# Performance work log

Hardware: AMD Instinct MI355X
Metric: run time of the kernel (lower is better)

Reference implementation:

```python
import jax, jax.numpy as jnp
import numpy as np

B, N, K = 128, 512, 6      # graphs, nodes per graph, kNN neighbors
IN_FEAT, POS_DIM, H = 128, 3, 256
NB = B * N                  # total nodes
EPS_BN = 1e-5


def setup_inputs() -> dict:
    key = jax.random.key(0)
    ks = jax.random.split(key, 32)
    inp = {
        "x": jax.random.normal(ks[0], (NB, IN_FEAT), dtype=jnp.float32),
        "pos": jax.random.normal(ks[1], (NB, POS_DIM), dtype=jnp.float32) * 5.0,
    }
    d_in = IN_FEAT + POS_DIM
    def lin(k, fi, fo):
        s = 1.0 / np.sqrt(fi)
        return jax.random.uniform(k, (fi, fo), jnp.float32, -s, s)
    # GCN layers
    inp["W1"] = lin(ks[2], d_in, H); inp["b1"] = jnp.zeros((H,), jnp.float32)
    inp["W2"] = lin(ks[3], H, H);    inp["b2"] = jnp.zeros((H,), jnp.float32)
    inp["W3"] = lin(ks[4], H, H);    inp["b3"] = jnp.zeros((H,), jnp.float32)
    # BatchNorm (eval mode: running stats)
    for i, km, kv in [(1, ks[5], ks[6]), (2, ks[7], ks[8]), (3, ks[9], ks[10])]:
        inp[f"g{i}"]  = jnp.ones((H,), jnp.float32)
        inp[f"be{i}"] = jnp.zeros((H,), jnp.float32)
        inp[f"m{i}"]  = jax.random.normal(km, (H,), jnp.float32) * 0.1
        inp[f"v{i}"]  = jax.random.uniform(kv, (H,), jnp.float32, 0.5, 1.5)
    # attention gate, heads
    inp["gate_w"] = lin(ks[11], H, 1); inp["gate_b"] = jnp.zeros((1,), jnp.float32)
    inp["aff_w"]  = lin(ks[12], H, 1); inp["aff_b"]  = jnp.zeros((1,), jnp.float32)
    inp["rl_w1"]  = lin(ks[13], H, H); inp["rl_b1"]  = jnp.zeros((H,), jnp.float32)
    inp["rl_w2"]  = lin(ks[14], H, POS_DIM); inp["rl_b2"] = jnp.zeros((POS_DIM,), jnp.float32)
    return inp


def _knn_edges(pos):
    # torch_geometric knn_graph semantics: per-graph k nearest neighbors,
    # no self loops, edges (neighbor -> node).  batch = repeat(arange(B), N).
    p = pos.reshape(B, N, POS_DIM)
    sq = jnp.sum(p * p, axis=-1)                                  # [B,N]
    d2 = sq[:, :, None] + sq[:, None, :] - 2.0 * jnp.einsum("bnd,bmd->bnm", p, p)
    d2 = jnp.where(jnp.eye(N, dtype=bool)[None], jnp.inf, d2)     # exclude self
    _, idx = jax.lax.top_k(-d2, K)                                # [B,N,K] local nbr ids
    offs = (jnp.arange(B) * N)[:, None, None]
    src = (idx + offs).reshape(-1)                                # neighbor (source)
    dst = jnp.repeat(jnp.arange(NB), K)                           # target node
    return src, dst


def _gcn(h, W, b, src, dst):
    # GCNConv: add self loops, symmetric norm D^-1/2 (A+I) D^-1/2
    hw = h @ W                                                    # [NB,H]
    deg = jax.ops.segment_sum(jnp.ones_like(dst, jnp.float32), dst, num_segments=NB) + 1.0
    dis = jax.lax.rsqrt(deg)
    norm = dis[src] * dis[dst]                                    # [E]
    agg = jax.ops.segment_sum(hw[src] * norm[:, None], dst, num_segments=NB)
    agg = agg + hw * (1.0 / deg)[:, None]                          # self loop term
    return agg + b


def _bn(h, g, be, m, v):
    return (h - m) * (g * jax.lax.rsqrt(v + EPS_BN)) + be


def reference(x, pos, W1, b1, W2, b2, W3, b3,
              g1, be1, m1, v1, g2, be2, m2, v2, g3, be3, m3, v3,
              gate_w, gate_b, aff_w, aff_b, rl_w1, rl_b1, rl_w2, rl_b2):
    src, dst = _knn_edges(pos)
    h = jnp.concatenate([x, pos], axis=1)                          # [NB, in_feat+3]
    h = jax.nn.relu(_bn(_gcn(h, W1, b1, src, dst), g1, be1, m1, v1))
    h = jax.nn.relu(_bn(_gcn(h, W2, b2, src, dst), g2, be2, m2, v2))
    h = jax.nn.relu(_bn(_gcn(h, W3, b3, src, dst), g3, be3, m3, v3))
    # (dropout is identity in eval mode)
    gate = jax.nn.relu(h @ gate_w + gate_b)[:, 0]                  # [NB]
    attn = jax.nn.softmax(gate.reshape(B, N), axis=1)              # scatter_softmax over batch
    gemb = jnp.einsum("bn,bnh->bh", attn, h.reshape(B, N, H))      # scatter_add of weighted x
    affinity = gemb @ aff_w + aff_b                                # [B,1]
    pose = jax.nn.relu(gemb @ rl_w1 + rl_b1) @ rl_w2 + rl_b2        # [B,3]
    return affinity, pose
```

## Files before the change

### kernel.cpp

```cpp
#include <hip/hip_runtime.h>
#include <hip/hip_bf16.h>
#include <math.h>
#include <float.h>

#define NBG 128
#define NND 512
#define KNN 6
#define NB_TOT (NBG*NND)
#define HF 256
#define NSTEP1 5

typedef short bf16x8 __attribute__((ext_vector_type(8)));
typedef float f32x4 __attribute__((ext_vector_type(4)));

__device__ __forceinline__ int swzoff(int row, int kbyte) {
    return (row*64 + kbyte) ^ (((row>>1)&3)<<4);
}

__device__ __forceinline__ void split_store(const float* v, char* hi_p, char* lo_p) {
    bf16x8 hi, lo;
    #pragma unroll
    for (int j = 0; j < 8; ++j) {
        __hip_bfloat16 h = __float2bfloat16(v[j]);
        float hf = __bfloat162float(h);
        __hip_bfloat16 l = __float2bfloat16(v[j] - hf);
        hi[j] = *(short*)&h;
        lo[j] = *(short*)&l;
    }
    *(bf16x8*)hi_p = hi;
    *(bf16x8*)lo_p = lo;
}

__device__ __forceinline__ int xcd_swz(int bid, int grid) {
    return (bid & 7) * (grid >> 3) + (bid >> 3);
}

__global__ __launch_bounds__(256) void knn_kernel(const float* __restrict__ pos,
                                                  unsigned short* __restrict__ nbr)
{
    const int blk = blockIdx.x;
    const int g = blk >> 3;
    const int chunk = (blk & 7) * 64;
    const int tid = threadIdx.x;
    const int node = chunk + (tid >> 2);
    const int sub = tid & 3;

    __shared__ float4 p4[NND + (NND>>6)];
    const float* pg = pos + (size_t)g * NND * 3;
    for (int n = tid; n < NND; n += 256) {
        float x = pg[n*3+0], y = pg[n*3+1], z = pg[n*3+2];
        p4[n + (n>>6)] = make_float4(x, y, z, x*x + y*y + z*z);
    }
    __syncthreads();

    const float4 pi = p4[node + (node>>6)];
    const float m2x = -2.0f*pi.x, m2y = -2.0f*pi.y, m2z = -2.0f*pi.z;

    float bdA[KNN], bdB[KNN]; int biA[KNN], biB[KNN];
    #pragma unroll
    for (int q = 0; q < KNN; ++q) {
        bdA[q] = FLT_MAX; biA[q] = 0x7fffffff;
        bdB[q] = FLT_MAX; biB[q] = 0x7fffffff;
    }

    const int j0 = sub * 128;
    const float4* baseA = &p4[sub*130];
    const float4* baseB = &p4[sub*130 + 65];

    #pragma unroll 2
    for (int t = 0; t < 64; ++t) {
        int ja = j0 + t, jb = j0 + 64 + t;
        float4 pa = baseA[t];
        float4 pb = baseB[t];
        float da = fmaf(m2z, pa.z, fmaf(m2y, pa.y, fmaf(m2x, pa.x, pa.w)));
        float db = fmaf(m2z, pb.z, fmaf(m2y, pb.y, fmaf(m2x, pb.x, pb.w)));
        da = (ja == node) ? FLT_MAX : da;
        db = (jb == node) ? FLT_MAX : db;
        float ca = da; int ia = ja;
        float cb = db; int ib = jb;
        #pragma unroll
        for (int q = 0; q < KNN; ++q) {
            bool sa = ca < bdA[q];
            float t1 = sa ? ca : bdA[q]; float t2 = sa ? bdA[q] : ca;
            int   t3 = sa ? ia : biA[q]; int   t4 = sa ? biA[q] : ia;
            bdA[q] = t1; ca = t2; biA[q] = t3; ia = t4;
            bool sb = cb < bdB[q];
            float u1 = sb ? cb : bdB[q]; float u2 = sb ? bdB[q] : cb;
            int   u3 = sb ? ib : biB[q]; int   u4 = sb ? biB[q] : ib;
            bdB[q] = u1; cb = u2; biB[q] = u3; ib = u4;
        }
    }

    float ld[KNN]; int li[KNN];
    #pragma unroll
    for (int q = 0; q < KNN; ++q) {
        float ad = bdA[q], xd = bdB[KNN-1-q];
        int   ai = biA[q], xi = biB[KNN-1-q];
        bool t = (ad < xd) || (ad == xd && ai < xi);
        ld[q] = t ? ad : xd;
        li[q] = t ? ai : xi;
    }
    #pragma unroll
    for (int pass = 0; pass < KNN-1; ++pass)
        #pragma unroll
        for (int a = 0; a < KNN-1-pass; ++a) {
            int b = a+1;
            bool sw = (ld[b] < ld[a]) || (ld[b] == ld[a] && li[b] < li[a]);
            float td = sw ? ld[b] : ld[a]; float ud = sw ? ld[a] : ld[b];
            int   ti = sw ? li[b] : li[a]; int   ui = sw ? li[a] : li[b];
            ld[a] = td; li[a] = ti; ld[b] = ud; li[b] = ui;
        }

    #pragma unroll
    for (int mi = 0; mi < 2; ++mi) {
        const int mask = 1 << mi;
        float od[KNN]; int oi[KNN];
        #pragma unroll
        for (int q = 0; q < KNN; ++q) {
            od[q] = __shfl_xor(ld[q], mask);
            oi[q] = __shfl_xor(li[q], mask);
        }
        #pragma unroll
        for (int q = 0; q < KNN; ++q) {
            float ad = ld[q], xd = od[KNN-1-q];
            int   ai = li[q], xi = oi[KNN-1-q];
            bool t = (ad < xd) || (ad == xd && ai < xi);
            ld[q] = t ? ad : xd;
            li[q] = t ? ai : xi;
        }
        #pragma unroll
        for (int pass = 0; pass < KNN-1; ++pass)
            #pragma unroll
            for (int a = 0; a < KNN-1-pass; ++a) {
                int b = a+1;
                bool sw = (ld[b] < ld[a]) || (ld[b] == ld[a] && li[b] < li[a]);
                float td = sw ? ld[b] : ld[a]; float ud = sw ? ld[a] : ld[b];
                int   ti = sw ? li[b] : li[a]; int   ui = sw ? li[a] : li[b];
                ld[a] = td; li[a] = ti; ld[b] = ud; li[b] = ui;
            }
    }

    if (sub == 0) {
        int base = (g*NND + node)*KNN;
        #pragma unroll
        for (int q = 0; q < KNN; ++q) nbr[base+q] = (unsigned short)li[q];
    }
}

__global__ __launch_bounds__(256) void prew_kernel(const float* __restrict__ W,
                                                   int K, int nstep,
                                                   char* __restrict__ Wimg)
{
    int gid = blockIdx.x*256 + threadIdx.x;
    int per_nb = nstep*512;
    int nb = gid / per_nb;
    int r  = gid - nb*per_nb;
    int step = r >> 9;
    int r2 = r & 511;
    int cl = r2 >> 2;
    int kc = (r2 & 3) * 8;
    float v[8];
    #pragma unroll
    for (int j = 0; j < 8; ++j) {
        int gk = step*32 + kc + j;
        v[j] = (gk < K) ? W[(size_t)gk*256 + nb*128 + cl] : 0.f;
    }
    char* base = Wimg + (size_t)nb*nstep*16384 + (size_t)step*16384;
    int off = swzoff(cl, kc*2);
    split_store(v, base + off, base + 8192 + off);
}

__global__ __launch_bounds__(256) void agg_first(const float* __restrict__ x,
                                                 const float* __restrict__ pos,
                                                 const unsigned short* __restrict__ nbr,
                                                 char* __restrict__ Aimg)
{
    int gid = xcd_swz(blockIdx.x, gridDim.x)*256 + threadIdx.x;
    int i = gid / 20, ch = gid - i*20;
    const float rs = 1.0f/sqrtf(7.0f);
    const float c1 = rs*rs, c2 = 1.0f/7.0f;
    const int gbase = i & ~(NND-1);
    float v[8];
    if (ch < 16) {
        int jn[KNN];
        #pragma unroll
        for (int q = 0; q < KNN; ++q) jn[q] = gbase + nbr[i*KNN+q];
        const float4* x4 = (const float4*)x;
        int c4 = ch*2;
        float4 s0 = x4[(size_t)i*32 + c4], s1 = x4[(size_t)i*32 + c4 + 1];
        float a0=0,a1=0,a2=0,a3=0,b0=0,b1=0,b2=0,b3=0;
        #pragma unroll
        for (int q = 0; q < KNN; ++q) {
            float4 t0 = x4[(size_t)jn[q]*32 + c4];
            float4 t1 = x4[(size_t)jn[q]*32 + c4 + 1];
            a0+=t0.x; a1+=t0.y; a2+=t0.z; a3+=t0.w;
            b0+=t1.x; b1+=t1.y; b2+=t1.z; b3+=t1.w;
        }
        v[0]=a0*c1+s0.x*c2; v[1]=a1*c1+s0.y*c2; v[2]=a2*c1+s0.z*c2; v[3]=a3*c1+s0.w*c2;
        v[4]=b0*c1+s1.x*c2; v[5]=b1*c1+s1.y*c2; v[6]=b2*c1+s1.z*c2; v[7]=b3*c1+s1.w*c2;
    } else if (ch == 16) {
        int jn[KNN];
        #pragma unroll
        for (int q = 0; q < KNN; ++q) jn[q] = gbase + nbr[i*KNN+q];
        float ax=0, ay=0, az=0;
        #pragma unroll
        for (int q = 0; q < KNN; ++q) {
            ax += pos[(size_t)jn[q]*3+0];
            ay += pos[(size_t)jn[q]*3+1];
            az += pos[(size_t)jn[q]*3+2];
        }
        v[0] = ax*c1 + pos[(size_t)i*3+0]*c2;
        v[1] = ay*c1 + pos[(size_t)i*3+1]*c2;
        v[2] = az*c1 + pos[(size_t)i*3+2]*c2;
        v[3]=v[4]=v[5]=v[6]=v[7]=0.f;
    } else {
        #pragma unroll
        for (int j = 0; j < 8; ++j) v[j] = 0.f;
    }
    int mb = i >> 7, row = i & 127, step = ch >> 2, kbyte = (ch & 3)*16;
    char* base = Aimg + (size_t)mb*(NSTEP1*16384) + (size_t)step*16384;
    int off = swzoff(row, kbyte);
    split_store(v, base + off, base + 8192 + off);
}

__global__ __launch_bounds__(256) void agg_h(const float* __restrict__ h,
                                             const unsigned short* __restrict__ nbr,
                                             char* __restrict__ Aimg)
{
    int gid = xcd_swz(blockIdx.x, gridDim.x)*256 + threadIdx.x;
    int i = gid >> 5, ch = gid & 31;
    const float rs = 1.0f/sqrtf(7.0f);
    const float c1 = rs*rs, c2 = 1.0f/7.0f;
    const int gbase = i & ~(NND-1);
    int jn[KNN];
    #pragma unroll
    for (int q = 0; q < KNN; ++q) jn[q] = gbase + nbr[i*KNN+q];
    const float4* h4 = (const float4*)h;
    int c4 = ch*2;
    float4 s0 = h4[(size_t)i*64 + c4], s1 = h4[(size_t)i*64 + c4 + 1];
    float a0=0,a1=0,a2=0,a3=0,b0=0,b1=0,b2=0,b3=0;
    #pragma unroll
    for (int q = 0; q < KNN; ++q) {
        float4 t0 = h4[(size_t)jn[q]*64 + c4];
        float4 t1 = h4[(size_t)jn[q]*64 + c4 + 1];
        a0+=t0.x; a1+=t0.y; a2+=t0.z; a3+=t0.w;
        b0+=t1.x; b1+=t1.y; b2+=t1.z; b3+=t1.w;
    }
    float v[8];
    v[0]=a0*c1+s0.x*c2; v[1]=a1*c1+s0.y*c2; v[2]=a2*c1+s0.z*c2; v[3]=a3*c1+s0.w*c2;
    v[4]=b0*c1+s1.x*c2; v[5]=b1*c1+s1.y*c2; v[6]=b2*c1+s1.z*c2; v[7]=b3*c1+s1.w*c2;
    int mb = i >> 7, row = i & 127, step = ch >> 2, kbyte = (ch & 3)*16;
    char* base = Aimg + (size_t)mb*(8*16384) + (size_t)step*16384;
    int off = swzoff(row, kbyte);
    split_store(v, base + off, base + 8192 + off);
}

__global__ __launch_bounds__(256,4) void gemm_mfma(
    const char* __restrict__ Aimg, const char* __restrict__ Wimg, int nstep,
    const float* __restrict__ bias,
    const float* __restrict__ gam, const float* __restrict__ bet,
    const float* __restrict__ mu,  const float* __restrict__ var,
    float* __restrict__ out)
{
    __shared__ uint4 lds4[34816/16];
    char* lds  = (char*)lds4;
    char* Alds = lds;
    char* Wlds = lds + 16384;
    float* scs = (float*)(lds + 32768);
    float* shs = scs + 256;
    const int tid = threadIdx.x;
    const int lane = tid & 63, wave = tid >> 6;
    const int wm = wave >> 1, wn = wave & 1;
    const int mblk = blockIdx.x, nblk = blockIdx.y;

    if (tid < 256) {
        float s = gam[tid] / sqrtf(var[tid] + 1e-5f);
        scs[tid] = s;
        shs[tid] = bet[tid] + (bias[tid] - mu[tid]) * s;
    }

    const char* Ab = Aimg + (size_t)mblk * nstep * 16384;
    const char* Wb = Wimg + (size_t)nblk * nstep * 16384;

    const char* gbase; char* lbase;
    int soff;
    if (wave < 2) { gbase = Ab;  lbase = Alds; soff = wave*8192; }
    else          { gbase = Wb;  lbase = Wlds; soff = (wave-2)*8192; }

    f32x4 acc[4][4];
    #pragma unroll
    for (int m = 0; m < 4; ++m)
        #pragma unroll
        for (int n = 0; n < 4; ++n) acc[m][n] = (f32x4){0.f,0.f,0.f,0.f};

    for (int s = 0; s < nstep; ++s) {
        #pragma unroll
        for (int i = 0; i < 8; ++i) {
            int off = soff + i*1024;
            __builtin_amdgcn_global_load_lds(
                (const __attribute__((address_space(1))) void*)(gbase + (size_t)s*16384 + off + lane*16),
                (__attribute__((address_space(3))) void*)(lbase + off), 16, 0, 0);
        }
        __syncthreads();
        const int kb = (lane >> 4) * 16;
        bf16x8 ah[4], al[4];
        #pragma unroll
        for (int m = 0; m < 4; ++m) {
            int row = wm*64 + m*16 + (lane & 15);
            int off = swzoff(row, kb);
            ah[m] = *(const bf16x8*)(Alds + off);
            al[m] = *(const bf16x8*)(Alds + 8192 + off);
        }
        #pragma unroll
        for (int n = 0; n < 4; ++n) {
            int col = wn*64 + n*16 + (lane & 15);
            int off = swzoff(col, kb);
            bf16x8 bh = *(const bf16x8*)(Wlds + off);
            bf16x8 bl = *(const bf16x8*)(Wlds + 8192 + off);
            #pragma unroll
            for (int m = 0; m < 4; ++m) {
                acc[m][n] = __builtin_amdgcn_mfma_f32_16x16x32_bf16(ah[m], bh, acc[m][n], 0, 0, 0);
                acc[m][n] = __builtin_amdgcn_mfma_f32_16x16x32_bf16(al[m], bh, acc[m][n], 0, 0, 0);
                acc[m][n] = __builtin_amdgcn_mfma_f32_16x16x32_bf16(ah[m], bl, acc[m][n], 0, 0, 0);
            }
        }
        __syncthreads();
    }

    #pragma unroll
    for (int n = 0; n < 4; ++n) {
        int c = nblk*128 + wn*64 + n*16 + (lane & 15);
        float sc = scs[c], sh = shs[c];
        #pragma unroll
        for (int m = 0; m < 4; ++m) {
            int r0 = mblk*128 + wm*64 + m*16 + (lane >> 4)*4;
            #pragma unroll
            for (int q = 0; q < 4; ++q) {
                float v = acc[m][n][q]*sc + sh;
                out[(size_t)(r0+q)*256 + c] = fmaxf(v, 0.f);
            }
        }
    }
}

__global__ __launch_bounds__(256) void gate_kernel(const float* __restrict__ h3,
                                                   const float* __restrict__ gate_w,
                                                   const float* __restrict__ gate_b,
                                                   float* __restrict__ gate)
{
    const int lane = threadIdx.x & 63;
    const int gw = (blockIdx.x*256 + threadIdx.x) >> 6;
    float4 w4 = ((const float4*)gate_w)[lane];
    float gb = gate_b[0];
    #pragma unroll
    for (int it = 0; it < 4; ++it) {
        int r = gw + it*8192;
        float4 v = ((const float4*)(h3 + (size_t)r*HF))[lane];
        float s = v.x*w4.x + v.y*w4.y + v.z*w4.z + v.w*w4.w;
        #pragma unroll
        for (int o = 32; o > 0; o >>= 1) s += __shfl_xor(s, o, 64);
        if (lane == 0) gate[r] = fmaxf(s + gb, 0.f);
    }
}

__device__ __forceinline__ float blk_sum256(float v, volatile float* red)
{
    #pragma unroll
    for (int o = 32; o > 0; o >>= 1) v += __shfl_xor(v, o, 64);
    __syncthreads();
    if ((threadIdx.x & 63) == 0) red[threadIdx.x >> 6] = v;
    __syncthreads();
    return (red[0] + red[1]) + (red[2] + red[3]);
}

__global__ __launch_bounds__(256) void attn_kernel(const float* __restrict__ gate,
                                                   float* __restrict__ attn)
{
    int g = blockIdx.x, tid = threadIdx.x;
    __shared__ float red[4];
    float g0 = gate[g*NND + tid];
    float g1 = gate[g*NND + 256 + tid];
    float m = fmaxf(g0, g1);
    #pragma unroll
    for (int o = 32; o > 0; o >>= 1) m = fmaxf(m, __shfl_xor(m, o, 64));
    if ((tid & 63) == 0) red[tid >> 6] = m;
    __syncthreads();
    m = fmaxf(fmaxf(red[0], red[1]), fmaxf(red[2], red[3]));
    float e0 = expf(g0 - m), e1 = expf(g1 - m);
    float S = blk_sum256(e0 + e1, red);
    attn[g*NND + tid]       = e0 / S;
    attn[g*NND + 256 + tid] = e1 / S;
}

__global__ __launch_bounds__(256) void gemb_kernel(const float* __restrict__ h3,
                                                   const float* __restrict__ attn,
                                                   float* __restrict__ gembp)
{
    const int g = blockIdx.x, s = blockIdx.y;
    const int tid = threadIdx.x, lane = tid & 63, w = tid >> 6;
    __shared__ float at[128];
    __shared__ float red4[4][HF];
    if (tid < 128) at[tid] = attn[g*NND + s*128 + tid];
    __syncthreads();
    const float* hb = h3 + (size_t)(g*NND + s*128 + w*32) * HF;
    float4 acc = make_float4(0.f, 0.f, 0.f, 0.f);
    #pragma unroll 4
    for (int n = 0; n < 32; ++n) {
        float a = at[w*32 + n];
        float4 v = ((const float4*)(hb + (size_t)n*HF))[lane];
        acc.x = fmaf(a, v.x, acc.x); acc.y = fmaf(a, v.y, acc.y);
        acc.z = fmaf(a, v.z, acc.z); acc.w = fmaf(a, v.w, acc.w);
    }
    *(float4*)&red4[w][lane*4] = acc;
    __syncthreads();
    if (tid < HF) {
        float sum = (red4[0][tid] + red4[1][tid]) + (red4[2][tid] + red4[3][tid]);
        gembp[((size_t)s*NBG + g)*HF + tid] = sum;
    }
}

__global__ __launch_bounds__(256) void heads_kernel(
    const float* __restrict__ gembp,
    const float* __restrict__ aff_w,  const float* __restrict__ aff_b,
    const float* __restrict__ rl_w1,  const float* __restrict__ rl_b1,
    const float* __restrict__ rl_w2,  const float* __restrict__ rl_b2,
    float* __restrict__ out)
{
    int g = blockIdx.x, tid = threadIdx.x;
    __shared__ float gemb[HF];
    __shared__ float red[4];
    float acc = (gembp[((size_t)0*NBG + g)*HF + tid] + gembp[((size_t)1*NBG + g)*HF + tid])
              + (gembp[((size_t)2*NBG + g)*HF + tid] + gembp[((size_t)3*NBG + g)*HF + tid]);
    gemb[tid] = acc;
    __syncthreads();

    float sa = blk_sum256(acc * aff_w[tid], red);
    if (tid == 0) out[g] = sa + aff_b[0];

    float t = rl_b1[tid];
    #pragma unroll 4
    for (int k2 = 0; k2 < HF; ++k2)
        t = fmaf(gemb[k2], rl_w1[(size_t)k2*HF + tid], t);
    t = fmaxf(t, 0.f);
    float s0 = blk_sum256(t * rl_w2[(size_t)tid*3 + 0], red);
    if (tid == 0) out[128 + g*3 + 0] = s0 + rl_b2[0];
    float s1 = blk_sum256(t * rl_w2[(size_t)tid*3 + 1], red);
    if (tid == 0) out[128 + g*3 + 1] = s1 + rl_b2[1];
    float s2 = blk_sum256(t * rl_w2[(size_t)tid*3 + 2], red);
    if (tid == 0) out[128 + g*3 + 2] = s2 + rl_b2[2];
}

extern "C" void kernel_launch(void* const* d_in, const int* in_sizes, int n_in,
                              void* d_out, int out_size, void* d_ws, size_t ws_size,
                              hipStream_t stream)
{
    const float* x      = (const float*)d_in[0];
    const float* pos    = (const float*)d_in[1];
    const float* W1     = (const float*)d_in[2];
    const float* b1     = (const float*)d_in[3];
    const float* W2     = (const float*)d_in[4];
    const float* b2     = (const float*)d_in[5];
    const float* W3     = (const float*)d_in[6];
    const float* b3     = (const float*)d_in[7];
    const float* g1     = (const float*)d_in[8];
    const float* be1    = (const float*)d_in[9];
    const float* m1     = (const float*)d_in[10];
    const float* v1     = (const float*)d_in[11];
    const float* g2     = (const float*)d_in[12];
    const float* be2    = (const float*)d_in[13];
    const float* m2     = (const float*)d_in[14];
    const float* v2     = (const float*)d_in[15];
    const float* g3     = (const float*)d_in[16];
    const float* be3    = (const float*)d_in[17];
    const float* m3     = (const float*)d_in[18];
    const float* v3     = (const float*)d_in[19];
    const float* gate_w = (const float*)d_in[20];
    const float* gate_b = (const float*)d_in[21];
    const float* aff_w  = (const float*)d_in[22];
    const float* aff_b  = (const float*)d_in[23];
    const float* rl_w1  = (const float*)d_in[24];
    const float* rl_b1  = (const float*)d_in[25];
    const float* rl_w2  = (const float*)d_in[26];
    const float* rl_b2  = (const float*)d_in[27];
    float* out = (float*)d_out;

    char* wsb = (char*)d_ws;
    unsigned short* nbr = (unsigned short*)wsb;
    char* Wimg1 = wsb + 786432;
    char* Wimg2 = Wimg1 + (size_t)2*NSTEP1*16384;
    char* Wimg3 = Wimg2 + (size_t)2*8*16384;
    float* h    = (float*)(Wimg3 + (size_t)2*8*16384);
    char* Aimg  = (char*)(h + (size_t)NB_TOT*HF);
    float* gate  = (float*)Aimg;
    float* attn  = gate + NB_TOT;
    float* gembp = attn + NB_TOT;

    knn_kernel<<<NBG*8, 256, 0, stream>>>(pos, nbr);
    prew_kernel<<<(2*NSTEP1*512)/256, 256, 0, stream>>>(W1, 131, NSTEP1, Wimg1);
    prew_kernel<<<(2*8*512)/256, 256, 0, stream>>>(W2, 256, 8, Wimg2);
    prew_kernel<<<(2*8*512)/256, 256, 0, stream>>>(W3, 256, 8, Wimg3);

    agg_first<<<(NB_TOT*20)/256, 256, 0, stream>>>(x, pos, nbr, Aimg);
    gemm_mfma<<<dim3(NB_TOT/128, 2), 256, 0, stream>>>(Aimg, Wimg1, NSTEP1,
        b1, g1, be1, m1, v1, h);
    agg_h<<<(NB_TOT*32)/256, 256, 0, stream>>>(h, nbr, Aimg);
    gemm_mfma<<<dim3(NB_TOT/128, 2), 256, 0, stream>>>(Aimg, Wimg2, 8,
        b2, g2, be2, m2, v2, h);
    agg_h<<<(NB_TOT*32)/256, 256, 0, stream>>>(h, nbr, Aimg);
    gemm_mfma<<<dim3(NB_TOT/128, 2), 256, 0, stream>>>(Aimg, Wimg3, 8,
        b3, g3, be3, m3, v3, h);

    gate_kernel<<<2048, 256, 0, stream>>>(h, gate_w, gate_b, gate);
    attn_kernel<<<NBG, 256, 0, stream>>>(gate, attn);
    gemb_kernel<<<dim3(NBG, 4), 256, 0, stream>>>(h, attn, gembp);
    heads_kernel<<<NBG, 256, 0, stream>>>(gembp, aff_w, aff_b,
                                          rl_w1, rl_b1, rl_w2, rl_b2, out);
}
```

Baseline: 248.0 us.

## Split kNN search over more threads, merge weight-prep launches, fuse softmax into gemb

The kNN kernel now gives each node 8 threads scanning 64 candidates each instead of 4 threads scanning 128, with one extra shuffle-merge round, and launches twice as many blocks. The three weight-prep launches become a single kernel that picks its matrix from the block index. The attention softmax kernel is removed and each gemb block recomputes the per-graph softmax from the gate values before the weighted sum. This is meant to cut launch count and shorten the serial kNN loop, at the cost of repeating the softmax in four blocks per graph and an extra merge round.

```diff
diff --git a/kernel.cpp b/kernel.cpp
--- a/kernel.cpp
+++ b/kernel.cpp
@@ -39,11 +39,11 @@
                                                   unsigned short* __restrict__ nbr)
 {
     const int blk = blockIdx.x;
-    const int g = blk >> 3;
-    const int chunk = (blk & 7) * 64;
+    const int g = blk >> 4;
+    const int chunk = (blk & 15) * 32;
     const int tid = threadIdx.x;
-    const int node = chunk + (tid >> 2);
-    const int sub = tid & 3;
+    const int node = chunk + (tid >> 3);
+    const int sub = tid & 7;
 
     __shared__ float4 p4[NND + (NND>>6)];
     const float* pg = pos + (size_t)g * NND * 3;
@@ -63,15 +63,14 @@
         bdB[q] = FLT_MAX; biB[q] = 0x7fffffff;
     }
 
-    const int j0 = sub * 128;
-    const float4* baseA = &p4[sub*130];
-    const float4* baseB = &p4[sub*130 + 65];
+    const int j0 = sub * 64;
+    const float4* base = &p4[sub*65];
 
     #pragma unroll 2
-    for (int t = 0; t < 64; ++t) {
-        int ja = j0 + t, jb = j0 + 64 + t;
-        float4 pa = baseA[t];
-        float4 pb = baseB[t];
+    for (int t = 0; t < 32; ++t) {
+        int ja = j0 + t, jb = j0 + 32 + t;
+        float4 pa = base[t];
+        float4 pb = base[t + 32];
         float da = fmaf(m2z, pa.z, fmaf(m2y, pa.y, fmaf(m2x, pa.x, pa.w)));
         float db = fmaf(m2z, pb.z, fmaf(m2y, pb.y, fmaf(m2x, pb.x, pb.w)));
         da = (ja == node) ? FLT_MAX : da;
@@ -112,7 +111,7 @@
         }
 
     #pragma unroll
-    for (int mi = 0; mi < 2; ++mi) {
+    for (int mi = 0; mi < 3; ++mi) {
         const int mask = 1 << mi;
         float od[KNN]; int oi[KNN];
         #pragma unroll
@@ -141,17 +140,23 @@
     }
 
     if (sub == 0) {
-        int base = (g*NND + node)*KNN;
-        #pragma unroll
-        for (int q = 0; q < KNN; ++q) nbr[base+q] = (unsigned short)li[q];
-    }
-}
-
-__global__ __launch_bounds__(256) void prew_kernel(const float* __restrict__ W,
-                                                   int K, int nstep,
-                                                   char* __restrict__ Wimg)
-{
-    int gid = blockIdx.x*256 + threadIdx.x;
+        int base2 = (g*NND + node)*KNN;
+        #pragma unroll
+        for (int q = 0; q < KNN; ++q) nbr[base2+q] = (unsigned short)li[q];
+    }
+}
+
+__global__ __launch_bounds__(256) void prew_all(
+    const float* __restrict__ W1, const float* __restrict__ W2,
+    const float* __restrict__ W3,
+    char* __restrict__ I1, char* __restrict__ I2, char* __restrict__ I3)
+{
+    int b = blockIdx.x;
+    const float* W; char* img; int K, nstep;
+    if (b < 20)      { W = W1; img = I1; K = 131; nstep = 5; }
+    else if (b < 52) { W = W2; img = I2; K = 256; nstep = 8; b -= 20; }
+    else             { W = W3; img = I3; K = 256; nstep = 8; b -= 52; }
+    int gid = b*256 + threadIdx.x;
     int per_nb = nstep*512;
     int nb = gid / per_nb;
     int r  = gid - nb*per_nb;
@@ -165,7 +170,7 @@
         int gk = step*32 + kc + j;
         v[j] = (gk < K) ? W[(size_t)gk*256 + nb*128 + cl] : 0.f;
     }
-    char* base = Wimg + (size_t)nb*nstep*16384 + (size_t)step*16384;
+    char* base = img + (size_t)nb*nstep*16384 + (size_t)step*16384;
     int off = swzoff(cl, kc*2);
     split_store(v, base + off, base + 8192 + off);
 }
@@ -373,35 +378,28 @@
     return (red[0] + red[1]) + (red[2] + red[3]);
 }
 
-__global__ __launch_bounds__(256) void attn_kernel(const float* __restrict__ gate,
-                                                   float* __restrict__ attn)
-{
-    int g = blockIdx.x, tid = threadIdx.x;
-    __shared__ float red[4];
-    float g0 = gate[g*NND + tid];
-    float g1 = gate[g*NND + 256 + tid];
-    float m = fmaxf(g0, g1);
-    #pragma unroll
-    for (int o = 32; o > 0; o >>= 1) m = fmaxf(m, __shfl_xor(m, o, 64));
-    if ((tid & 63) == 0) red[tid >> 6] = m;
-    __syncthreads();
-    m = fmaxf(fmaxf(red[0], red[1]), fmaxf(red[2], red[3]));
-    float e0 = expf(g0 - m), e1 = expf(g1 - m);
-    float S = blk_sum256(e0 + e1, red);
-    attn[g*NND + tid]       = e0 / S;
-    attn[g*NND + 256 + tid] = e1 / S;
-}
-
 __global__ __launch_bounds__(256) void gemb_kernel(const float* __restrict__ h3,
-                                                   const float* __restrict__ attn,
+                                                   const float* __restrict__ gate,
                                                    float* __restrict__ gembp)
 {
     const int g = blockIdx.x, s = blockIdx.y;
     const int tid = threadIdx.x, lane = tid & 63, w = tid >> 6;
     __shared__ float at[128];
     __shared__ float red4[4][HF];
-    if (tid < 128) at[tid] = attn[g*NND + s*128 + tid];
-    __syncthreads();
+    __shared__ float red[4];
+
+    float g0 = gate[g*NND + tid];
+    float g1 = gate[g*NND + 256 + tid];
+    float m = fmaxf(g0, g1);
+    #pragma unroll
+    for (int o = 32; o > 0; o >>= 1) m = fmaxf(m, __shfl_xor(m, o, 64));
+    if ((tid & 63) == 0) red[tid >> 6] = m;
+    __syncthreads();
+    m = fmaxf(fmaxf(red[0], red[1]), fmaxf(red[2], red[3]));
+    float S = blk_sum256(expf(g0 - m) + expf(g1 - m), red);
+    if (tid < 128) at[tid] = expf(gate[g*NND + s*128 + tid] - m) / S;
+    __syncthreads();
+
     const float* hb = h3 + (size_t)(g*NND + s*128 + w*32) * HF;
     float4 acc = make_float4(0.f, 0.f, 0.f, 0.f);
     #pragma unroll 4
@@ -492,13 +490,10 @@
     float* h    = (float*)(Wimg3 + (size_t)2*8*16384);
     char* Aimg  = (char*)(h + (size_t)NB_TOT*HF);
     float* gate  = (float*)Aimg;
-    float* attn  = gate + NB_TOT;
-    float* gembp = attn + NB_TOT;
-
-    knn_kernel<<<NBG*8, 256, 0, stream>>>(pos, nbr);
-    prew_kernel<<<(2*NSTEP1*512)/256, 256, 0, stream>>>(W1, 131, NSTEP1, Wimg1);
-    prew_kernel<<<(2*8*512)/256, 256, 0, stream>>>(W2, 256, 8, Wimg2);
-    prew_kernel<<<(2*8*512)/256, 256, 0, stream>>>(W3, 256, 8, Wimg3);
+    float* gembp = gate + NB_TOT;
+
+    knn_kernel<<<NBG*16, 256, 0, stream>>>(pos, nbr);
+    prew_all<<<84, 256, 0, stream>>>(W1, W2, W3, Wimg1, Wimg2, Wimg3);
 
     agg_first<<<(NB_TOT*20)/256, 256, 0, stream>>>(x, pos, nbr, Aimg);
     gemm_mfma<<<dim3(NB_TOT/128, 2), 256, 0, stream>>>(Aimg, Wimg1, NSTEP1,
@@ -511,8 +506,7 @@
         b3, g3, be3, m3, v3, h);
 
     gate_kernel<<<2048, 256, 0, stream>>>(h, gate_w, gate_b, gate);
-    attn_kernel<<<NBG, 256, 0, stream>>>(gate, attn);
-    gemb_kernel<<<dim3(NBG, 4), 256, 0, stream>>>(h, attn, gembp);
+    gemb_kernel<<<dim3(NBG, 4), 256, 0, stream>>>(h, gate, gembp);
     heads_kernel<<<NBG, 256, 0, stream>>>(gembp, aff_w, aff_b,
                                           rl_w1, rl_b1, rl_w2, rl_b2, out);
 }
```

Result: no change. 249.4 us (+0.6%).
